# Optimization experiments

Measured on AMD Instinct MI355X. Metric: run time of the kernel, lower is better.

Reference implementation:

```python
import jax, jax.numpy as jnp
import numpy as np
from jax import lax


def _conv1(y, w):
    # y: (B, C) channel vector; w: (3,) Conv1d kernel (cross-correlation, pad=1, no bias)
    yp = jnp.pad(y, ((0, 0), (1, 1)))
    return w[0] * yp[:, :-2] + w[1] * yp[:, 1:-1] + w[2] * yp[:, 2:]


def _scale_branch(xs, dw_w, dw_b, ca_w, ra_w, gate_w, gate_b):
    # xs: (B, C, h, w) one scale of the multi-scale token map
    B, C = xs.shape[0], xs.shape[1]
    xs = lax.conv_general_dilated(
        xs, dw_w, (1, 1), 'SAME', feature_group_count=C,
        dimension_numbers=('NCHW', 'OIHW', 'NCHW')) + dw_b[None, :, None, None]
    avg = xs.mean(axis=(2, 3))          # (B, C) == AdaptiveAvgPool2d(1)
    mx = xs.max(axis=(2, 3))            # (B, C) == AdaptiveMaxPool2d(1)
    gw = jax.nn.softmax(avg @ gate_w + gate_b, axis=1)  # (B, 2) gating over experts
    pooled = avg + mx
    ca_s = jax.nn.sigmoid(_conv1(pooled, ca_w))          # CA channel gate
    ra_s = 1.0 - jax.nn.sigmoid(_conv1(pooled, ra_w))    # RA reverse gate
    # blend the two SE-style experts per channel, then broadcast-multiply
    scale = gw[:, 0:1] * ca_s + gw[:, 1:2] * ra_s        # (B, C)
    out = xs * scale[:, :, None, None]
    return out.reshape(B, C, -1).transpose(0, 2, 1)      # (B, h*w, C)


def setup_inputs() -> dict:
    key = jax.random.key(0)
    ks = jax.random.split(key, 12)
    B, N, Cin, Ch = 8, 5376, 384, 768
    s = lambda k, shape, fan: jax.random.normal(k, shape, jnp.float32) * (1.0 / np.sqrt(fan))
    return {
        'x': jax.random.normal(ks[0], (B, N, Cin), jnp.float32),
        'fc1_w': s(ks[1], (Cin, Ch), Cin),
        'fc1_b': jnp.zeros((Ch,), jnp.float32),
        'dw_w': s(ks[2], (Ch, 1, 3, 3), 9),
        'dw_b': jnp.zeros((Ch,), jnp.float32),
        'ca_w': s(ks[3], (3,), 3),
        'ra_w': s(ks[4], (3,), 3),
        'gate_w': s(ks[5], (Ch, 2), Ch),
        'gate_b': jnp.zeros((2,), jnp.float32),
        'fc2_w': s(ks[6], (Ch, Cin), Ch),
        'fc2_b': jnp.zeros((Cin,), jnp.float32),
        'H': 32,
        'W': 32,
    }


def reference(x, fc1_w, fc1_b, dw_w, dw_b, ca_w, ra_w, gate_w, gate_b, fc2_w, fc2_b, H, W):
    B, N, _ = x.shape
    C = fc1_w.shape[1]
    h = x @ fc1_w + fc1_b                     # fc1: (B, N, C)
    n = N // 21
    to_map = lambda seg, hh, ww: seg.transpose(0, 2, 1).reshape(B, C, hh, ww)
    x1 = to_map(h[:, :16 * n], 2 * H, 2 * W)
    x2 = to_map(h[:, 16 * n:20 * n], H, W)
    x3 = to_map(h[:, 20 * n:], H // 2, W // 2)
    parts = [_scale_branch(xi, dw_w, dw_b, ca_w, ra_w, gate_w, gate_b)
             for xi in (x1, x2, x3)]
    h = jnp.concatenate(parts, axis=1)        # (B, N, C)
    h = jax.nn.gelu(h, approximate=False)     # torch nn.GELU default = exact erf
    return h @ fc2_w + fc2_b
```

## Files before the change

kernel.cpp:

```cpp
#include <hip/hip_runtime.h>
#include <hip/hip_bf16.h>
#include <math.h>

#define B_   8
#define NTOK 5376
#define CIN  384
#define CH   768
#define M_   (B_*NTOK)

typedef unsigned short u16;
typedef unsigned int   u32;

using bf16x8 = __attribute__((ext_vector_type(8))) short;
using bf16x2 = __attribute__((ext_vector_type(2))) short;
using f32x4  = __attribute__((ext_vector_type(4))) float;

__device__ __forceinline__ u16 f2bf(float f) {
    union { float f; u32 u; } v; v.f = f;
    u32 r = v.u + 0x7fffu + ((v.u >> 16) & 1u);
    return (u16)(r >> 16);
}
__device__ __forceinline__ float bf2f(u16 u) {
    union { u32 u; float f; } v; v.u = ((u32)u) << 16;
    return v.f;
}
__device__ __forceinline__ u32 fkey(float f) {
    union { float f; u32 u; } v; v.f = f;
    return (v.u & 0x80000000u) ? ~v.u : (v.u | 0x80000000u);
}
__device__ __forceinline__ float fkeyinv(u32 k) {
    union { u32 u; float f; } v;
    v.u = (k & 0x80000000u) ? (k ^ 0x80000000u) : ~k;
    return v.f;
}
__device__ __forceinline__ float gelu_exact(float f) {
    return 0.5f * f * (1.f + erff(f * 0.70710678118654752f));
}

__global__ void k_cvt_wT(const float* __restrict__ w, u16* __restrict__ wT, int K, int N) {
    int i = blockIdx.x * blockDim.x + threadIdx.x;
    if (i >= N * K) return;
    int n = i / K, k = i % K;
    wT[i] = f2bf(w[k * N + n]);
}

#define BM 128
#define BN 128
#define BK 64

template<int AM, bool OUT_BF16>
__launch_bounds__(256)
__global__ void gemm_fused(const void* __restrict__ Asrc, const u16* __restrict__ Bt,
                           const float* __restrict__ bias, void* __restrict__ Cout,
                           int M, int N, int K) {
    __shared__ __align__(16) u16 sA[BM * BK];
    __shared__ __align__(16) u16 sB[BN * BK];
    const int mt = blockIdx.x, nt = blockIdx.y;
    const int tid = threadIdx.x;
    const int wave = tid >> 6, lane = tid & 63;
    const int wm = wave >> 1, wn = wave & 1;
    const int row0 = mt * BM, col0 = nt * BN;
    const int lr = lane & 15, lk = lane >> 4;

    f32x4 acc[4][4];
#pragma unroll
    for (int m = 0; m < 4; m++)
#pragma unroll
        for (int n = 0; n < 4; n++) acc[m][n] = (f32x4){0.f, 0.f, 0.f, 0.f};

    const int KT = K / BK;
    for (int kt = 0; kt < KT; ++kt) {
        const int k0 = kt * BK;
#pragma unroll
        for (int it = 0; it < 4; ++it) {
            int g  = it * 256 + tid;
            int r  = g >> 3;
            int ks = g & 7;
            const u16* gB = Bt + (size_t)(col0 + r) * K + k0 + ks * 8;
            u16* lB = sB + (size_t)(it * 256 + wave * 64) * 8;
            __builtin_amdgcn_global_load_lds(
                (const __attribute__((address_space(1))) u32*)(const void*)gB,
                (__attribute__((address_space(3))) u32*)(void*)lB, 16, 0, 0);
            if (AM == 2) {
                const u16* gA = (const u16*)Asrc + (size_t)(row0 + r) * K + k0 + ks * 8;
                u16* lA = sA + (size_t)(it * 256 + wave * 64) * 8;
                __builtin_amdgcn_global_load_lds(
                    (const __attribute__((address_space(1))) u32*)(const void*)gA,
                    (__attribute__((address_space(3))) u32*)(void*)lA, 16, 0, 0);
            }
        }
        if (AM == 0) {
#pragma unroll
            for (int it = 0; it < 4; ++it) {
                int g  = it * 256 + tid;
                int r  = g >> 3;
                int ks = g & 7;
                const float* ga = (const float*)Asrc + (size_t)(row0 + r) * K + k0 + ks * 8;
                float4 a0 = ((const float4*)ga)[0];
                float4 a1 = ((const float4*)ga)[1];
                union { __hip_bfloat162 h2[4]; bf16x8 v; } o;
                o.h2[0] = __float22bfloat162_rn({a0.x, a0.y});
                o.h2[1] = __float22bfloat162_rn({a0.z, a0.w});
                o.h2[2] = __float22bfloat162_rn({a1.x, a1.y});
                o.h2[3] = __float22bfloat162_rn({a1.z, a1.w});
                *(bf16x8*)&sA[(size_t)g * 8] = o.v;
            }
        }
        __syncthreads();
#pragma unroll
        for (int kk = 0; kk < 2; ++kk) {
            bf16x8 af[4], bfr[4];
#pragma unroll
            for (int m = 0; m < 4; m++)
                af[m] = *(const bf16x8*)&sA[(wm * 64 + m * 16 + lr) * BK + kk * 32 + lk * 8];
#pragma unroll
            for (int n = 0; n < 4; n++)
                bfr[n] = *(const bf16x8*)&sB[(wn * 64 + n * 16 + lr) * BK + kk * 32 + lk * 8];
#pragma unroll
            for (int m = 0; m < 4; m++)
#pragma unroll
                for (int n = 0; n < 4; n++)
                    acc[m][n] = __builtin_amdgcn_mfma_f32_16x16x32_bf16(af[m], bfr[n], acc[m][n], 0, 0, 0);
        }
        __syncthreads();
    }

#pragma unroll
    for (int m = 0; m < 4; m++) {
#pragma unroll
        for (int n = 0; n < 4; n++) {
            int col = col0 + wn * 64 + n * 16 + lr;
            float bv = bias[col];
#pragma unroll
            for (int r = 0; r < 4; r++) {
                int row = row0 + wm * 64 + m * 16 + lk * 4 + r;
                float v = acc[m][n][r] + bv;
                if (OUT_BF16)
                    ((u16*)Cout)[(size_t)row * N + col] = f2bf(v);
                else
                    ((float*)Cout)[(size_t)row * N + col] = v;
            }
        }
    }
}

__launch_bounds__(384)
__global__ void k_conv(const u16* __restrict__ h, const float* __restrict__ dw_w,
                       const float* __restrict__ dw_b, u16* __restrict__ xs,
                       float* __restrict__ psum, u32* __restrict__ pmaxk) {
    const int tile = blockIdx.x, b = blockIdx.y;
    int s, xt, yt, tokbase, LW;
    if (tile < 64)      { s = 0; xt = tile & 7;  yt = tile >> 3; tokbase = 0;    LW = 6; }
    else if (tile < 80) { int u = tile - 64; s = 1; xt = u & 3; yt = u >> 2; tokbase = 4096; LW = 5; }
    else                { int u = tile - 80; s = 2; xt = u & 1; yt = u >> 1; tokbase = 5120; LW = 4; }
    const int W = 1 << LW, H = W;
    const int x0 = xt * 8, y0 = yt * 8;
    const int c0 = threadIdx.x * 2;

    float wv[9][2], dwb[2];
#pragma unroll
    for (int j = 0; j < 2; j++) {
        dwb[j] = dw_b[c0 + j];
#pragma unroll
        for (int t = 0; t < 9; t++) wv[t][j] = dw_w[(c0 + j) * 9 + t];
    }

    const size_t base = ((size_t)(b * NTOK + tokbase)) * CH + c0;
    const bf16x2 z2 = (bf16x2){0, 0};
    bool colv[10];
    int coloff[10];
#pragma unroll
    for (int j = 0; j < 10; j++) {
        int xx = x0 - 1 + j;
        colv[j] = (xx >= 0) && (xx < W);
        coloff[j] = xx * CH;
    }

    bf16x2 r[3][10];

#define LOADROW(slot, yrow) {                                                   \
        int yr_ = (yrow);                                                       \
        bool rv_ = ((unsigned)yr_ < (unsigned)H);                               \
        int rb_ = yr_ * W * CH;                                                 \
        _Pragma("unroll")                                                       \
        for (int j = 0; j < 10; j++)                                            \
            r[slot][j] = (rv_ && colv[j]) ? *(const bf16x2*)&h[base + rb_ + coloff[j]] : z2; \
    }

    LOADROW(0, y0 - 1);
    LOADROW(1, y0);

    float as[2] = {0.f, 0.f};
    float am[2] = {-3.4e38f, -3.4e38f};

#pragma unroll
    for (int yy = 0; yy < 8; ++yy) {
        const int sm1 = yy % 3, sc = (yy + 1) % 3, sp1 = (yy + 2) % 3;
        LOADROW(sp1, y0 + yy + 1);
        const int orow = (y0 + yy) * W * CH;
#pragma unroll
        for (int p = 0; p < 8; ++p) {
            float o[2];
#pragma unroll
            for (int j = 0; j < 2; j++) o[j] = dwb[j];
#pragma unroll
            for (int kx = 0; kx < 3; ++kx) {
                const int ci = p + kx;
#pragma unroll
                for (int j = 0; j < 2; j++) {
                    o[j] += wv[0 + kx][j] * bf2f((u16)r[sm1][ci][j]);
                    o[j] += wv[3 + kx][j] * bf2f((u16)r[sc ][ci][j]);
                    o[j] += wv[6 + kx][j] * bf2f((u16)r[sp1][ci][j]);
                }
            }
            bf16x2 ov;
#pragma unroll
            for (int j = 0; j < 2; j++) {
                ov[j] = (short)f2bf(o[j]);
                as[j] += o[j];
                am[j] = fmaxf(am[j], o[j]);
            }
            *(bf16x2*)&xs[base + orow + (x0 + p) * CH] = ov;
        }
    }
#undef LOADROW

#pragma unroll
    for (int j = 0; j < 2; j++) {
        atomicAdd(&psum[(s * 8 + b) * CH + c0 + j], as[j]);
        atomicMax(&pmaxk[(s * 8 + b) * CH + c0 + j], fkey(am[j]));
    }
}

__global__ void k_scale(const float* __restrict__ psum, const u32* __restrict__ pmaxk,
                        const float* __restrict__ gate_w, const float* __restrict__ gate_b,
                        const float* __restrict__ ca_w, const float* __restrict__ ra_w,
                        float* __restrict__ scale) {
    int s = blockIdx.x, b = blockIdx.y;
    int tid = threadIdx.x;
    float npos = (s == 0) ? 4096.f : (s == 1) ? 1024.f : 256.f;
    __shared__ float pooled[CH];
    __shared__ float rl[4][2];
    float l0 = 0.f, l1 = 0.f;
#pragma unroll
    for (int j = 0; j < 3; j++) {
        int c = j * 256 + tid;
        size_t idx = ((size_t)s * 8 + b) * CH + c;
        float avg = psum[idx] / npos;
        float mxv = fkeyinv(pmaxk[idx]);
        pooled[c] = avg + mxv;
        l0 += avg * gate_w[c * 2 + 0];
        l1 += avg * gate_w[c * 2 + 1];
    }
    for (int off = 32; off; off >>= 1) {
        l0 += __shfl_down(l0, off);
        l1 += __shfl_down(l1, off);
    }
    int wave = tid >> 6, lane = tid & 63;
    if (lane == 0) { rl[wave][0] = l0; rl[wave][1] = l1; }
    __syncthreads();
    float L0 = rl[0][0] + rl[1][0] + rl[2][0] + rl[3][0] + gate_b[0];
    float L1 = rl[0][1] + rl[1][1] + rl[2][1] + rl[3][1] + gate_b[1];
    float mxl = fmaxf(L0, L1);
    float e0 = expf(L0 - mxl), e1 = expf(L1 - mxl);
    float g0 = e0 / (e0 + e1), g1 = e1 / (e0 + e1);
    float cw0 = ca_w[0], cw1 = ca_w[1], cw2 = ca_w[2];
    float rw0 = ra_w[0], rw1 = ra_w[1], rw2 = ra_w[2];
#pragma unroll
    for (int j = 0; j < 3; j++) {
        int c = j * 256 + tid;
        float pm = (c > 0)      ? pooled[c - 1] : 0.f;
        float pc = pooled[c];
        float pp = (c < CH - 1) ? pooled[c + 1] : 0.f;
        float cas = 1.f / (1.f + expf(-(cw0 * pm + cw1 * pc + cw2 * pp)));
        float ras = 1.f - 1.f / (1.f + expf(-(rw0 * pm + rw1 * pc + rw2 * pp)));
        scale[((size_t)s * 8 + b) * CH + c] = g0 * cas + g1 * ras;
    }
}

#define NG (M_ * (CH / 8))
__global__ void k_apply(u16* __restrict__ xs, const float* __restrict__ scale) {
    for (int gi = blockIdx.x * blockDim.x + threadIdx.x; gi < NG;
         gi += gridDim.x * blockDim.x) {
        int c8 = gi % 96;
        int tl = gi / 96;
        int t = tl % NTOK, b = tl / NTOK;
        int s = (t < 4096) ? 0 : (t < 5120 ? 1 : 2);
        const float4* sp = (const float4*)&scale[((size_t)(s * 8 + b)) * CH + c8 * 8];
        float4 sc0 = sp[0], sc1 = sp[1];
        float scv[8] = {sc0.x, sc0.y, sc0.z, sc0.w, sc1.x, sc1.y, sc1.z, sc1.w};
        bf16x8 v = *(const bf16x8*)&xs[(size_t)gi * 8];
        bf16x8 o;
#pragma unroll
        for (int j = 0; j < 8; j++) {
            float f = bf2f((u16)v[j]) * scv[j];
            o[j] = (short)f2bf(gelu_exact(f));
        }
        *(bf16x8*)&xs[(size_t)gi * 8] = o;
    }
}

extern "C" void kernel_launch(void* const* d_in, const int* in_sizes, int n_in,
                              void* d_out, int out_size, void* d_ws, size_t ws_size,
                              hipStream_t stream) {
    const float* x      = (const float*)d_in[0];
    const float* fc1_w  = (const float*)d_in[1];
    const float* fc1_b  = (const float*)d_in[2];
    const float* dw_w   = (const float*)d_in[3];
    const float* dw_b   = (const float*)d_in[4];
    const float* ca_w   = (const float*)d_in[5];
    const float* ra_w   = (const float*)d_in[6];
    const float* gate_w = (const float*)d_in[7];
    const float* gate_b = (const float*)d_in[8];
    const float* fc2_w  = (const float*)d_in[9];
    const float* fc2_b  = (const float*)d_in[10];

    char* ws = (char*)d_ws;
    u16*  hb    = (u16*)(ws);
    u16*  xs    = (u16*)(ws + 66060288);
    u16*  w1T   = (u16*)(ws + 132120576);
    u16*  w2T   = (u16*)(ws + 132710400);
    float* psum = (float*)(ws + 133300224);
    u32*  pmaxk = (u32*)(ws + 133373952);
    float* scale= (float*)(ws + 133447680);

    hipMemsetAsync((void*)psum, 0, 147456, stream);

    k_cvt_wT<<<(CIN * CH + 255) / 256, 256, 0, stream>>>(fc1_w, w1T, CIN, CH);
    k_cvt_wT<<<(CIN * CH + 255) / 256, 256, 0, stream>>>(fc2_w, w2T, CH, CIN);

    gemm_fused<0, true><<<dim3(M_ / BM, CH / BN), 256, 0, stream>>>(
        (const void*)x, w1T, fc1_b, (void*)hb, M_, CH, CIN);

    k_conv<<<dim3(84, 8), 384, 0, stream>>>(hb, dw_w, dw_b, xs, psum, pmaxk);

    k_scale<<<dim3(3, 8), 256, 0, stream>>>(psum, pmaxk, gate_w, gate_b, ca_w, ra_w, scale);

    k_apply<<<4096, 256, 0, stream>>>(xs, scale);

    gemm_fused<2, false><<<dim3(M_ / BM, CIN / BN), 256, 0, stream>>>(
        (const void*)xs, w2T, fc2_b, d_out, M_, CIN, CH);
}
```

Before: 365.2 us.

## Double-buffer GEMM LDS tiles and retile depthwise conv for wider channel loads

The GEMM now keeps two LDS buffers for the A and B tiles. Each iteration prefetches the next K-tile, through async global-to-LDS loads and register-staged fp32 A loads, while MFMAs run on the current tile, and one barrier per iteration is removed. This is meant to hide global memory latency behind compute. The depthwise conv kernel now has each thread handle 4 channels with 8-byte loads over 4-wide spatial tiles, using 192 threads and twice as many blocks, to improve load width and occupancy. The trade-offs are double the LDS use per GEMM block, more register pressure, and more halo reloading in the conv.

```diff
diff --git a/kernel.cpp b/kernel.cpp
--- a/kernel.cpp
+++ b/kernel.cpp
@@ -12,7 +12,7 @@
 typedef unsigned int   u32;
 
 using bf16x8 = __attribute__((ext_vector_type(8))) short;
-using bf16x2 = __attribute__((ext_vector_type(2))) short;
+using bf16x4 = __attribute__((ext_vector_type(4))) short;
 using f32x4  = __attribute__((ext_vector_type(4))) float;
 
 __device__ __forceinline__ u16 f2bf(float f) {
@@ -53,8 +53,8 @@
 __global__ void gemm_fused(const void* __restrict__ Asrc, const u16* __restrict__ Bt,
                            const float* __restrict__ bias, void* __restrict__ Cout,
                            int M, int N, int K) {
-    __shared__ __align__(16) u16 sA[BM * BK];
-    __shared__ __align__(16) u16 sB[BN * BK];
+    __shared__ __align__(16) u16 sA[2][BM * BK];
+    __shared__ __align__(16) u16 sB[2][BN * BK];
     const int mt = blockIdx.x, nt = blockIdx.y;
     const int tid = threadIdx.x;
     const int wave = tid >> 6, lane = tid & 63;
@@ -68,8 +68,9 @@
 #pragma unroll
         for (int n = 0; n < 4; n++) acc[m][n] = (f32x4){0.f, 0.f, 0.f, 0.f};
 
-    const int KT = K / BK;
-    for (int kt = 0; kt < KT; ++kt) {
+    float4 a0[4], a1[4];
+
+    auto STAGE_DMA = [&](int buf, int kt) {
         const int k0 = kt * BK;
 #pragma unroll
         for (int it = 0; it < 4; ++it) {
@@ -77,52 +78,75 @@
             int r  = g >> 3;
             int ks = g & 7;
             const u16* gB = Bt + (size_t)(col0 + r) * K + k0 + ks * 8;
-            u16* lB = sB + (size_t)(it * 256 + wave * 64) * 8;
+            u16* lB = sB[buf] + (size_t)(it * 256 + wave * 64) * 8;
             __builtin_amdgcn_global_load_lds(
                 (const __attribute__((address_space(1))) u32*)(const void*)gB,
                 (__attribute__((address_space(3))) u32*)(void*)lB, 16, 0, 0);
             if (AM == 2) {
                 const u16* gA = (const u16*)Asrc + (size_t)(row0 + r) * K + k0 + ks * 8;
-                u16* lA = sA + (size_t)(it * 256 + wave * 64) * 8;
+                u16* lA = sA[buf] + (size_t)(it * 256 + wave * 64) * 8;
                 __builtin_amdgcn_global_load_lds(
                     (const __attribute__((address_space(1))) u32*)(const void*)gA,
                     (__attribute__((address_space(3))) u32*)(void*)lA, 16, 0, 0);
             }
         }
-        if (AM == 0) {
-#pragma unroll
-            for (int it = 0; it < 4; ++it) {
-                int g  = it * 256 + tid;
-                int r  = g >> 3;
-                int ks = g & 7;
-                const float* ga = (const float*)Asrc + (size_t)(row0 + r) * K + k0 + ks * 8;
-                float4 a0 = ((const float4*)ga)[0];
-                float4 a1 = ((const float4*)ga)[1];
-                union { __hip_bfloat162 h2[4]; bf16x8 v; } o;
-                o.h2[0] = __float22bfloat162_rn({a0.x, a0.y});
-                o.h2[1] = __float22bfloat162_rn({a0.z, a0.w});
-                o.h2[2] = __float22bfloat162_rn({a1.x, a1.y});
-                o.h2[3] = __float22bfloat162_rn({a1.z, a1.w});
-                *(bf16x8*)&sA[(size_t)g * 8] = o.v;
-            }
-        }
-        __syncthreads();
+    };
+    auto ALOAD = [&](int kt) {
+        const int k0 = kt * BK;
+#pragma unroll
+        for (int it = 0; it < 4; ++it) {
+            int g  = it * 256 + tid;
+            int r  = g >> 3;
+            int ks = g & 7;
+            const float* ga = (const float*)Asrc + (size_t)(row0 + r) * K + k0 + ks * 8;
+            a0[it] = ((const float4*)ga)[0];
+            a1[it] = ((const float4*)ga)[1];
+        }
+    };
+    auto ASTORE = [&](int buf) {
+#pragma unroll
+        for (int it = 0; it < 4; ++it) {
+            int g = it * 256 + tid;
+            union { __hip_bfloat162 h2[4]; bf16x8 v; } o;
+            o.h2[0] = __float22bfloat162_rn({a0[it].x, a0[it].y});
+            o.h2[1] = __float22bfloat162_rn({a0[it].z, a0[it].w});
+            o.h2[2] = __float22bfloat162_rn({a1[it].x, a1[it].y});
+            o.h2[3] = __float22bfloat162_rn({a1[it].z, a1[it].w});
+            *(bf16x8*)&sA[buf][(size_t)g * 8] = o.v;
+        }
+    };
+
+    STAGE_DMA(0, 0);
+    if (AM == 0) { ALOAD(0); ASTORE(0); }
+    __syncthreads();
+
+    const int KT = K / BK;
+    int cur = 0;
+    for (int kt = 0; kt < KT; ++kt) {
+        const int nxt = cur ^ 1;
+        const bool more = (kt + 1 < KT);
+        if (more) {
+            if (AM == 0) ALOAD(kt + 1);
+            STAGE_DMA(nxt, kt + 1);
+        }
 #pragma unroll
         for (int kk = 0; kk < 2; ++kk) {
             bf16x8 af[4], bfr[4];
 #pragma unroll
             for (int m = 0; m < 4; m++)
-                af[m] = *(const bf16x8*)&sA[(wm * 64 + m * 16 + lr) * BK + kk * 32 + lk * 8];
+                af[m] = *(const bf16x8*)&sA[cur][(wm * 64 + m * 16 + lr) * BK + kk * 32 + lk * 8];
 #pragma unroll
             for (int n = 0; n < 4; n++)
-                bfr[n] = *(const bf16x8*)&sB[(wn * 64 + n * 16 + lr) * BK + kk * 32 + lk * 8];
+                bfr[n] = *(const bf16x8*)&sB[cur][(wn * 64 + n * 16 + lr) * BK + kk * 32 + lk * 8];
 #pragma unroll
             for (int m = 0; m < 4; m++)
 #pragma unroll
                 for (int n = 0; n < 4; n++)
                     acc[m][n] = __builtin_amdgcn_mfma_f32_16x16x32_bf16(af[m], bfr[n], acc[m][n], 0, 0, 0);
         }
+        if (more && AM == 0) ASTORE(nxt);
         __syncthreads();
+        cur = nxt;
     }
 
 #pragma unroll
@@ -144,54 +168,54 @@
     }
 }
 
-__launch_bounds__(384)
+__launch_bounds__(192, 3)
 __global__ void k_conv(const u16* __restrict__ h, const float* __restrict__ dw_w,
                        const float* __restrict__ dw_b, u16* __restrict__ xs,
                        float* __restrict__ psum, u32* __restrict__ pmaxk) {
     const int tile = blockIdx.x, b = blockIdx.y;
     int s, xt, yt, tokbase, LW;
-    if (tile < 64)      { s = 0; xt = tile & 7;  yt = tile >> 3; tokbase = 0;    LW = 6; }
-    else if (tile < 80) { int u = tile - 64; s = 1; xt = u & 3; yt = u >> 2; tokbase = 4096; LW = 5; }
-    else                { int u = tile - 80; s = 2; xt = u & 1; yt = u >> 1; tokbase = 5120; LW = 4; }
+    if (tile < 128)      { s = 0; xt = tile & 15; yt = tile >> 4; tokbase = 0;    LW = 6; }
+    else if (tile < 160) { int u = tile - 128; s = 1; xt = u & 7; yt = u >> 3; tokbase = 4096; LW = 5; }
+    else                 { int u = tile - 160; s = 2; xt = u & 3; yt = u >> 2; tokbase = 5120; LW = 4; }
     const int W = 1 << LW, H = W;
-    const int x0 = xt * 8, y0 = yt * 8;
-    const int c0 = threadIdx.x * 2;
-
-    float wv[9][2], dwb[2];
-#pragma unroll
-    for (int j = 0; j < 2; j++) {
+    const int x0 = xt * 4, y0 = yt * 8;
+    const int c0 = threadIdx.x * 4;
+
+    float wv[9][4], dwb[4];
+#pragma unroll
+    for (int j = 0; j < 4; j++) {
         dwb[j] = dw_b[c0 + j];
 #pragma unroll
         for (int t = 0; t < 9; t++) wv[t][j] = dw_w[(c0 + j) * 9 + t];
     }
 
     const size_t base = ((size_t)(b * NTOK + tokbase)) * CH + c0;
-    const bf16x2 z2 = (bf16x2){0, 0};
-    bool colv[10];
-    int coloff[10];
-#pragma unroll
-    for (int j = 0; j < 10; j++) {
+    const bf16x4 z4 = (bf16x4){0, 0, 0, 0};
+    bool colv[6];
+    int coloff[6];
+#pragma unroll
+    for (int j = 0; j < 6; j++) {
         int xx = x0 - 1 + j;
         colv[j] = (xx >= 0) && (xx < W);
         coloff[j] = xx * CH;
     }
 
-    bf16x2 r[3][10];
+    bf16x4 r[3][6];
 
 #define LOADROW(slot, yrow) {                                                   \
         int yr_ = (yrow);                                                       \
         bool rv_ = ((unsigned)yr_ < (unsigned)H);                               \
         int rb_ = yr_ * W * CH;                                                 \
         _Pragma("unroll")                                                       \
-        for (int j = 0; j < 10; j++)                                            \
-            r[slot][j] = (rv_ && colv[j]) ? *(const bf16x2*)&h[base + rb_ + coloff[j]] : z2; \
+        for (int j = 0; j < 6; j++)                                             \
+            r[slot][j] = (rv_ && colv[j]) ? *(const bf16x4*)&h[base + rb_ + coloff[j]] : z4; \
     }
 
     LOADROW(0, y0 - 1);
     LOADROW(1, y0);
 
-    float as[2] = {0.f, 0.f};
-    float am[2] = {-3.4e38f, -3.4e38f};
+    float as[4] = {0.f, 0.f, 0.f, 0.f};
+    float am[4] = {-3.4e38f, -3.4e38f, -3.4e38f, -3.4e38f};
 
 #pragma unroll
     for (int yy = 0; yy < 8; ++yy) {
@@ -199,34 +223,34 @@
         LOADROW(sp1, y0 + yy + 1);
         const int orow = (y0 + yy) * W * CH;
 #pragma unroll
-        for (int p = 0; p < 8; ++p) {
-            float o[2];
-#pragma unroll
-            for (int j = 0; j < 2; j++) o[j] = dwb[j];
+        for (int p = 0; p < 4; ++p) {
+            float o[4];
+#pragma unroll
+            for (int j = 0; j < 4; j++) o[j] = dwb[j];
 #pragma unroll
             for (int kx = 0; kx < 3; ++kx) {
                 const int ci = p + kx;
 #pragma unroll
-                for (int j = 0; j < 2; j++) {
+                for (int j = 0; j < 4; j++) {
                     o[j] += wv[0 + kx][j] * bf2f((u16)r[sm1][ci][j]);
                     o[j] += wv[3 + kx][j] * bf2f((u16)r[sc ][ci][j]);
                     o[j] += wv[6 + kx][j] * bf2f((u16)r[sp1][ci][j]);
                 }
             }
-            bf16x2 ov;
-#pragma unroll
-            for (int j = 0; j < 2; j++) {
+            bf16x4 ov;
+#pragma unroll
+            for (int j = 0; j < 4; j++) {
                 ov[j] = (short)f2bf(o[j]);
                 as[j] += o[j];
                 am[j] = fmaxf(am[j], o[j]);
             }
-            *(bf16x2*)&xs[base + orow + (x0 + p) * CH] = ov;
+            *(bf16x4*)&xs[base + orow + (x0 + p) * CH] = ov;
         }
     }
 #undef LOADROW
 
 #pragma unroll
-    for (int j = 0; j < 2; j++) {
+    for (int j = 0; j < 4; j++) {
         atomicAdd(&psum[(s * 8 + b) * CH + c0 + j], as[j]);
         atomicMax(&pmaxk[(s * 8 + b) * CH + c0 + j], fkey(am[j]));
     }
@@ -332,7 +356,7 @@
     gemm_fused<0, true><<<dim3(M_ / BM, CH / BN), 256, 0, stream>>>(
         (const void*)x, w1T, fc1_b, (void*)hb, M_, CH, CIN);
 
-    k_conv<<<dim3(84, 8), 384, 0, stream>>>(hb, dw_w, dw_b, xs, psum, pmaxk);
+    k_conv<<<dim3(168, 8), 192, 0, stream>>>(hb, dw_w, dw_b, xs, psum, pmaxk);
 
     k_scale<<<dim3(3, 8), 256, 0, stream>>>(psum, pmaxk, gate_w, gate_b, ca_w, ra_w, scale);
 
```

After: 363.4 us. Within noise of the previous version (-0.5%).
